# Kernel optimization log

Measured on AMD Instinct MI355X. Metric: run time of the kernel, lower is better.

The kernel has to match this reference:

```python
import jax, jax.numpy as jnp
import numpy as np


def _conv(x, w, b, dilation=1):
    # NHWC input, HWIO kernel, SAME padding, optional dilation (TF Conv2D semantics)
    y = jax.lax.conv_general_dilated(
        x, w, window_strides=(1, 1), padding='SAME',
        rhs_dilation=(dilation, dilation),
        dimension_numbers=('NHWC', 'HWIO', 'NHWC'))
    return y + b


def _grid_pool(x, row_loc, col_loc):
    # Irregular-grid mean pool + broadcast back (tf resize of a 1x1 cell == broadcast).
    # Vectorized as two normalized one-hot contractions instead of per-cell loops.
    B, H, W, C = x.shape
    M = row_loc.shape[0] - 1
    N = col_loc.shape[0] - 1
    row_ids = jnp.searchsorted(row_loc, jnp.arange(H), side='right') - 1  # [H] in [0,M)
    col_ids = jnp.searchsorted(col_loc, jnp.arange(W), side='right') - 1  # [W] in [0,N)
    Rm = jax.nn.one_hot(row_ids, M, dtype=x.dtype).T            # [M,H]
    Cm = jax.nn.one_hot(col_ids, N, dtype=x.dtype)              # [W,N]
    Rm = Rm / jnp.sum(Rm, axis=1, keepdims=True)                # row-mean weights
    Cm = Cm / jnp.sum(Cm, axis=0, keepdims=True)                # col-mean weights
    pooled = jnp.einsum('mh,bhwc,wn->bmnc', Rm, x, Cm)          # per-cell means [B,M,N,C]
    return pooled[:, row_ids][:, :, col_ids]                    # broadcast back [B,H,W,C]


def setup_inputs() -> dict:
    key = jax.random.key(0)
    ks = jax.random.split(key, 8)
    B, H, W, Cin = 2, 1024, 1024, 18
    inp = {
        'input': jax.random.normal(ks[0], (B, H, W, Cin), dtype=jnp.float32),
        'row_loc': (jnp.arange(17, dtype=jnp.int32) * (H // 16)),  # 16 irregular-capable cells, endpoints 0..H
        'col_loc': (jnp.arange(17, dtype=jnp.int32) * (W // 16)),
        'w1': jax.random.normal(ks[1], (3, 3, Cin, 6), dtype=jnp.float32) * 0.1,
        'b1': jnp.zeros((6,), jnp.float32),
        'w2': jax.random.normal(ks[2], (3, 3, Cin, 6), dtype=jnp.float32) * 0.1,
        'b2': jnp.zeros((6,), jnp.float32),
        'w3': jax.random.normal(ks[3], (3, 3, Cin, 6), dtype=jnp.float32) * 0.1,
        'b3': jnp.zeros((6,), jnp.float32),
        'wb1': jax.random.normal(ks[4], (1, 1, 18, 18), dtype=jnp.float32) * 0.1,
        'bb1': jnp.zeros((18,), jnp.float32),
        'wb2': jax.random.normal(ks[5], (1, 1, 18, 1), dtype=jnp.float32) * 0.1,
        'bb2': jnp.zeros((1,), jnp.float32),
    }
    return inp


def reference(input, row_loc, col_loc, w1, b1, w2, b2, w3, b3, wb1, bb1, wb2, bb2):
    c1 = jax.nn.relu(_conv(input, w1, b1, 1))
    c2 = jax.nn.relu(_conv(input, w2, b2, 2))
    c3 = jax.nn.relu(_conv(input, w3, b3, 3))
    c = jnp.concatenate([c1, c2, c3], axis=3)          # [B,H,W,18]
    branch1 = jax.nn.relu(_conv(c, wb1, bb1, 1))       # [B,H,W,18]
    branch1 = _grid_pool(branch1, row_loc, col_loc)
    branch2 = _conv(c, wb2, bb2, 1)                    # [B,H,W,1]
    branch2 = _grid_pool(branch2, row_loc, col_loc)
    branch2 = jax.nn.sigmoid(branch2)
    output = jnp.concatenate([branch1, c, branch2], axis=3)  # [B,H,W,37]
    return (output, branch2)
```

## Files before the change

kernel.cpp:

```cpp
#include <hip/hip_runtime.h>
#include <math.h>

typedef _Float16 f16;
typedef _Float16 f16x2 __attribute__((ext_vector_type(2)));
typedef _Float16 f16x8 __attribute__((ext_vector_type(8)));
typedef float    f32x4 __attribute__((ext_vector_type(4)));

static constexpr int B = 2, H = 1024, W = 1024;
static constexpr int NCELL = 16;
static constexpr unsigned TOTAL1 = 2u*1024u*1024u*37u;

static constexpr int TR = 16, TC = 32;
static constexpr int SR = TR + 6;
static constexpr int SC = TC + 6;
static constexpr int NTILE = B*(H/TR)*(W/TC);

static constexpr size_t WT_OFF   = 0;
static constexpr size_t WBT_OFF  = 21504;
static constexpr size_t BIAS_OFF = 23552;
static constexpr size_t CWS_OFF  = 32768;
static constexpr size_t SUMS_OFF = CWS_OFF + (size_t)NTILE*18432;
static constexpr size_t P1_OFF   = SUMS_OFF + 9728*4;
static constexpr size_t P2_OFF   = P1_OFF + 9216*4;
static constexpr size_t RID_OFF  = P2_OFF + 512*4;
static constexpr size_t CID_OFF  = RID_OFF + 1024*4;

__device__ __forceinline__ int cell_of(const int* __restrict__ loc, int x) {
    int id = 0;
#pragma unroll
    for (int i = 1; i < NCELL; ++i) id = (loc[i] <= x) ? i : id;
    return id;
}

__global__ __launch_bounds__(256)
void prep(const float* __restrict__ w1, const float* __restrict__ b1,
          const float* __restrict__ w2, const float* __restrict__ b2,
          const float* __restrict__ w3, const float* __restrict__ b3,
          const float* __restrict__ wb1, const float* __restrict__ bb1,
          const float* __restrict__ wb2, const float* __restrict__ bb2,
          f16* __restrict__ wT, f16* __restrict__ wbT, float* __restrict__ biasPad,
          float* __restrict__ sums)
{
    const int tid = threadIdx.x;
    for (int t = tid; t < 9728; t += 256) sums[t] = 0.f;
    for (int t = tid; t < 10752; t += 256) {
        int cv = t / 3584, r = t - cv*3584;
        int co = r / 224,  k = r - co*224;
        float val = 0.f;
        if (k < 216 && co < 6) {
            int tap = k / 24, ci = k - tap*24;
            if (ci < 18) {
                const float* wsrc = cv==0 ? w1 : cv==1 ? w2 : w3;
                val = wsrc[(tap*18 + ci)*6 + co];
            }
        }
        wT[t] = (f16)val;
    }
    for (int t = tid; t < 1024; t += 256) {
        int nt = t >> 9, r = t & 511;
        int colv = r >> 5, ci = r & 31;
        int co2 = nt*16 + colv;
        float val = 0.f;
        if (ci < 18) {
            if (co2 < 18) val = wb1[ci*18 + co2];
            else if (co2 == 18) val = wb2[ci];
        }
        wbT[t] = (f16)val;
    }
    for (int t = tid; t < 80; t += 256) {
        float val = 0.f;
        if (t < 48) { int cv = t >> 4, co = t & 15;
            const float* bp = cv==0 ? b1 : cv==1 ? b2 : b3;
            val = (co < 6) ? bp[co] : 0.f; }
        else if (t < 64) val = bb1[t - 48];
        else { int c = t - 64;
            val = (c==0) ? bb1[16] : (c==1) ? bb1[17] : (c==2) ? bb2[0] : 0.f; }
        biasPad[t] = val;
    }
}

__global__ __launch_bounds__(512)
void conv_mfma(const float* __restrict__ in,
               const f16* __restrict__ wT, const f16* __restrict__ wbT,
               const float* __restrict__ biasPad,
               const int* __restrict__ row_loc, const int* __restrict__ col_loc,
               f16* __restrict__ c_ws, float* __restrict__ sums)
{
    __shared__ __align__(16) f16 s_a[SR*SC*24];
    __shared__ float s_red[8][19];

    const int tid = threadIdx.x;
    const int bx  = blockIdx.x;
    const int b   = bx >> 11, rem = bx & 2047;
    const int h0  = (rem >> 5) * TR, w0 = (rem & 31) * TC;

    const int gh0 = h0 - 3, gw0 = w0 - 3;
    const bool interior = (gh0 >= 0) && (h0 + TR + 3 <= H) && (gw0 >= 0) && (w0 + TC + 3 <= W);
#pragma unroll
    for (int k = 0; k < 2; ++k) {
        const int p = tid + k*512;
        if (p < SR*SC) {
            const int r = p / SC, cc = p - r*SC;
            const int gh = gh0 + r, gw = gw0 + cc;
            const bool ok = interior || ((unsigned)gh < (unsigned)H && (unsigned)gw < (unsigned)W);
            float2 L[9];
            if (ok) {
                const float* sp = in + ((size_t)((size_t)b*H + gh)*W + gw)*18;
#pragma unroll
                for (int j = 0; j < 9; ++j) L[j] = *(const float2*)(sp + 2*j);
            } else {
#pragma unroll
                for (int j = 0; j < 9; ++j) L[j] = make_float2(0.f, 0.f);
            }
            f16x8 A0, A1, A2;
#pragma unroll
            for (int j = 0; j < 4; ++j) { A0[2*j] = (f16)L[j].x;   A0[2*j+1] = (f16)L[j].y; }
#pragma unroll
            for (int j = 0; j < 4; ++j) { A1[2*j] = (f16)L[4+j].x; A1[2*j+1] = (f16)L[4+j].y; }
            A2[0] = (f16)L[8].x; A2[1] = (f16)L[8].y;
#pragma unroll
            for (int j = 2; j < 8; ++j) A2[j] = (f16)0.f;
            *(f16x8*)&s_a[p*24 + 0]  = A0;
            *(f16x8*)&s_a[p*24 + 8]  = A1;
            *(f16x8*)&s_a[p*24 + 16] = A2;
        }
    }
    __syncthreads();

    const int lane = tid & 63, wv = tid >> 6;
    const int lm = lane & 15, g = lane >> 4;
    const int rq = wv & 3, ch2 = wv >> 2;

    f32x4 acc[3][4];
#pragma unroll
    for (int cv = 0; cv < 3; ++cv)
#pragma unroll
        for (int mt = 0; mt < 4; ++mt) acc[cv][mt] = (f32x4){0.f,0.f,0.f,0.f};

#pragma unroll
    for (int cv = 0; cv < 3; ++cv) {
        const int d = cv + 1;
        const f16* wtc = wT + cv*3584 + lm*224 + g*8;
        f16x8 bf[7];
#pragma unroll
        for (int kb = 0; kb < 7; ++kb) bf[kb] = *(const f16x8*)(wtc + kb*32);
        int tofs[7];
#pragma unroll
        for (int kb = 0; kb < 7; ++kb) {
            int i8 = kb*4 + g; if (i8 > 26) i8 = 26;
            int tap = i8 / 3;
            int ci0 = (i8 - tap*3) * 8;
            int ky = tap / 3, kx = tap - ky*3;
            tofs[kb] = (((ky-1)*d)*SC + (kx-1)*d)*24 + ci0;
        }
#pragma unroll
        for (int mt = 0; mt < 4; ++mt) {
            const int py = rq*4 + mt;
            const int base = ((py + 3)*SC + ch2*16 + lm + 3) * 24;
            f32x4 a = acc[cv][mt];
#pragma unroll
            for (int kb = 0; kb < 7; ++kb) {
                f16x8 af = *(const f16x8*)&s_a[base + tofs[kb]];
                a = __builtin_amdgcn_mfma_f32_16x16x32_f16(af, bf[kb], a, 0, 0, 0);
            }
            acc[cv][mt] = a;
        }
    }

    __syncthreads();
    f16* ct = s_a;
    const float bs0 = biasPad[lm], bs1 = biasPad[16 + lm], bs2 = biasPad[32 + lm];
    const bool act = (lm < 6);
#pragma unroll
    for (int cv = 0; cv < 3; ++cv) {
        const float bv = cv==0 ? bs0 : cv==1 ? bs1 : bs2;
#pragma unroll
        for (int mt = 0; mt < 4; ++mt) {
            const int py = rq*4 + mt;
#pragma unroll
            for (int r = 0; r < 4; ++r) {
                float val = fmaxf(acc[cv][mt][r] + bv, 0.f);
                const int px = ch2*16 + g*4 + r;
                if (act) ct[(py*TC + px)*18 + cv*6 + lm] = (f16)val;
            }
        }
    }
    __syncthreads();

    {
        const f16x8* src = (const f16x8*)ct;
        f16x8* dst = (f16x8*)(c_ws + (size_t)bx * 9216);
#pragma unroll
        for (int k = 0; k < 3; ++k) {
            const int i = tid + k*512;
            if (i < 1152) dst[i] = src[i];
        }
    }

    const f16x8 wbf0 = *(const f16x8*)(wbT + lm*32 + g*8);
    const f16x8 wbf1 = *(const f16x8*)(wbT + (16 + lm)*32 + g*8);
    const f32x4 z4 = (f32x4){0.f,0.f,0.f,0.f};
    const unsigned* ctu = (const unsigned*)ct;
    f32x4 acc2[4][2];
#pragma unroll
    for (int mt = 0; mt < 4; ++mt) {
        const int py = rq*4 + mt;
        const int p = py*TC + ch2*16 + lm;
        const int du = (p*36 + g*16) >> 2;
        union { f16x8 v; unsigned u[4]; } A;
#pragma unroll
        for (int j = 0; j < 4; ++j) A.u[j] = ctu[du + j];
        acc2[mt][0] = __builtin_amdgcn_mfma_f32_16x16x32_f16(A.v, wbf0, z4, 0, 0, 0);
        acc2[mt][1] = __builtin_amdgcn_mfma_f32_16x16x32_f16(A.v, wbf1, z4, 0, 0, 0);
    }

    const float bb0 = biasPad[48 + lm];
    const float bb1v = biasPad[64 + lm];
    const int rid0 = cell_of(row_loc, h0), rid1 = cell_of(row_loc, h0 + TR - 1);
    const int cid0 = cell_of(col_loc, w0), cid1 = cell_of(col_loc, w0 + TC - 1);
    if (rid0 == rid1 && cid0 == cid1) {
        float ps0 = 0.f, ps1 = 0.f;
#pragma unroll
        for (int mt = 0; mt < 4; ++mt)
#pragma unroll
            for (int r = 0; r < 4; ++r) {
                float v0 = fmaxf(acc2[mt][0][r] + bb0, 0.f);
                float t1 = acc2[mt][1][r] + bb1v;
                float v1x = (lm < 2) ? fmaxf(t1, 0.f) : t1;
                ps0 += v0; ps1 += v1x;
            }
        ps0 += __shfl_xor(ps0, 16); ps0 += __shfl_xor(ps0, 32);
        ps1 += __shfl_xor(ps1, 16); ps1 += __shfl_xor(ps1, 32);
        if (lane < 16) s_red[wv][lane] = ps0;
        if (lane < 3)  s_red[wv][16 + lane] = ps1;
        __syncthreads();
        if (tid < 19) {
            float s = 0.f;
#pragma unroll
            for (int wvi = 0; wvi < 8; ++wvi) s += s_red[wvi][tid];
            const int cell = b*256 + rid0*16 + cid0;
            atomicAdd(&sums[cell*19 + tid], s);
        }
    } else {
#pragma unroll
        for (int mt = 0; mt < 4; ++mt) {
            const int py = rq*4 + mt;
            const int rid = cell_of(row_loc, h0 + py);
#pragma unroll
            for (int r = 0; r < 4; ++r) {
                const int px = ch2*16 + g*4 + r;
                const int cell = b*256 + rid*16 + cell_of(col_loc, w0 + px);
                float v0 = fmaxf(acc2[mt][0][r] + bb0, 0.f);
                atomicAdd(&sums[cell*19 + lm], v0);
                if (lm < 3) {
                    float t1 = acc2[mt][1][r] + bb1v;
                    float v1x = (lm < 2) ? fmaxf(t1, 0.f) : t1;
                    atomicAdd(&sums[cell*19 + 16 + lm], v1x);
                }
            }
        }
    }
}

__global__ __launch_bounds__(256)
void finalize(const int* __restrict__ row_loc, const int* __restrict__ col_loc,
              const float* __restrict__ sums,
              float* __restrict__ pooled1, float* __restrict__ pooled2,
              int* __restrict__ row_ids, int* __restrict__ col_ids)
{
    __shared__ int rcnt[NCELL], ccnt[NCELL];
    const int tid = threadIdx.x;
    if (tid < NCELL) { rcnt[tid] = 0; ccnt[tid] = 0; }
    __syncthreads();
    for (int h = tid; h < H; h += 256) {
        int r = cell_of(row_loc, h); row_ids[h] = r; atomicAdd(&rcnt[r], 1);
    }
    for (int w = tid; w < W; w += 256) {
        int cc = cell_of(col_loc, w); col_ids[w] = cc; atomicAdd(&ccnt[cc], 1);
    }
    __syncthreads();
    for (int t = tid; t < B*256*18; t += 256) {
        int cell = t / 18, ch = t - cell*18;
        int rid = (cell >> 4) & 15, cid = cell & 15;
        int cnt = rcnt[rid] * ccnt[cid];
        pooled1[t] = (cnt > 0) ? sums[cell*19 + ch] / (float)cnt : 0.f;
    }
    for (int t = tid; t < B*256; t += 256) {
        int rid = (t >> 4) & 15, cid = t & 15;
        int cnt = rcnt[rid] * ccnt[cid];
        float v = (cnt > 0) ? sums[t*19 + 18] / (float)cnt : 0.f;
        pooled2[t] = 1.f / (1.f + __expf(-v));
    }
}

__global__ __launch_bounds__(256)
void assemble(const f16* __restrict__ c_ws, const float* __restrict__ pooled1,
              const float* __restrict__ pooled2, const int* __restrict__ row_ids,
              const int* __restrict__ col_ids, float* __restrict__ out)
{
    __shared__ __align__(16) f16 s_c[1024*18];
    __shared__ float s_p1[16*18];
    __shared__ float s_p2[16];
    __shared__ unsigned char s_cid[1024];

    const int tid = threadIdx.x;
    const int bx  = blockIdx.x;
    const int b   = bx >> 10, h = bx & 1023;

    const int tbase = b*2048 + (h >> 4)*32;
    const size_t rofs = (size_t)(h & 15) * 1152;
    const char* cbase = (const char*)c_ws;
    float4* dstv = (float4*)s_c;
#pragma unroll
    for (int k = 0; k < 9; ++k) {
        const int j = tid + k*256;
        const int t = j / 72, i = j - t*72;
        const float4 v = *(const float4*)(cbase + (size_t)(tbase + t)*18432 + rofs + (size_t)i*16);
        dstv[j] = v;
    }
    const int rid = row_ids[h];
    for (int i = tid; i < 288; i += 256) {
        int cid = i / 18, ch = i - cid*18;
        s_p1[i] = pooled1[((size_t)(b*256 + rid*16 + cid))*18 + ch];
    }
    if (tid < 16) s_p2[tid] = pooled2[b*256 + rid*16 + tid];
    for (int i = tid; i < 1024; i += 256) s_cid[i] = (unsigned char)col_ids[i];
    __syncthreads();

    float* orow = out + (size_t)bx * (1024*37);
    for (int i4 = tid; i4 < 1024*37/4; i4 += 256) {
        const int o0 = i4*4;
        float v[4];
#pragma unroll
        for (int j = 0; j < 4; ++j) {
            const int o = o0 + j;
            const unsigned pix = (unsigned)o / 37u;
            const int ch = o - (int)pix*37;
            const int cid = s_cid[pix];
            float val;
            if (ch < 18)       val = s_p1[cid*18 + ch];
            else if (ch < 36)  val = (float)s_c[pix*18 + (ch - 18)];
            else               val = s_p2[cid];
            v[j] = val;
        }
        *(float4*)(orow + o0) = make_float4(v[0], v[1], v[2], v[3]);
    }
    float* o2 = out + (size_t)TOTAL1 + (size_t)bx * 1024;
    {
        const int p0 = tid * 4;
        float4 v = make_float4(s_p2[s_cid[p0]], s_p2[s_cid[p0+1]],
                               s_p2[s_cid[p0+2]], s_p2[s_cid[p0+3]]);
        *(float4*)(o2 + p0) = v;
    }
}

extern "C" void kernel_launch(void* const* d_in, const int* in_sizes, int n_in,
                              void* d_out, int out_size, void* d_ws, size_t ws_size,
                              hipStream_t stream)
{
    (void)in_sizes; (void)n_in; (void)out_size; (void)ws_size;
    const float* in      = (const float*)d_in[0];
    const int*   row_loc = (const int*)d_in[1];
    const int*   col_loc = (const int*)d_in[2];
    const float *w1 = (const float*)d_in[3],  *b1  = (const float*)d_in[4];
    const float *w2 = (const float*)d_in[5],  *b2  = (const float*)d_in[6];
    const float *w3 = (const float*)d_in[7],  *b3  = (const float*)d_in[8];
    const float *wb1= (const float*)d_in[9],  *bb1 = (const float*)d_in[10];
    const float *wb2= (const float*)d_in[11], *bb2 = (const float*)d_in[12];

    float* out = (float*)d_out;
    char*  ws  = (char*)d_ws;

    f16*   wT      = (f16*)(ws + WT_OFF);
    f16*   wbT     = (f16*)(ws + WBT_OFF);
    float* biasPad = (float*)(ws + BIAS_OFF);
    f16*   c_ws    = (f16*)(ws + CWS_OFF);
    float* sums    = (float*)(ws + SUMS_OFF);
    float* pooled1 = (float*)(ws + P1_OFF);
    float* pooled2 = (float*)(ws + P2_OFF);
    int*   row_ids = (int*)(ws + RID_OFF);
    int*   col_ids = (int*)(ws + CID_OFF);

    prep<<<dim3(1), dim3(256), 0, stream>>>(w1, b1, w2, b2, w3, b3,
                                            wb1, bb1, wb2, bb2, wT, wbT, biasPad, sums);

    conv_mfma<<<dim3(NTILE), dim3(512), 0, stream>>>(
        in, wT, wbT, biasPad, row_loc, col_loc, c_ws, sums);

    finalize<<<dim3(1), dim3(256), 0, stream>>>(
        row_loc, col_loc, sums, pooled1, pooled2, row_ids, col_ids);

    assemble<<<dim3(B*H), dim3(256), 0, stream>>>(
        c_ws, pooled1, pooled2, row_ids, col_ids, out);
}
```

Baseline: 214.1 us.

## Fuse pooling and output assembly into per-cell conv blocks with fallback flag

Each block now owns one full 64x64 grid cell, processed in four 16-row strips. When the cell matches the uniform grid, the block computes the cell mean in-block and writes the final 37-channel output and branch2 directly. It sets a flag only when a block hits irregular cells; finalize and assemble exit early when the flag is clear. This removes the separate assemble pass (reading c_ws back and writing the output) in the common case. The cost is only 512 blocks of 1024 threads with sequential strips, which may reduce latency hiding and occupancy.

```diff
diff --git a/kernel.cpp b/kernel.cpp
--- a/kernel.cpp
+++ b/kernel.cpp
@@ -10,20 +10,16 @@
 static constexpr int NCELL = 16;
 static constexpr unsigned TOTAL1 = 2u*1024u*1024u*37u;
 
-static constexpr int TR = 16, TC = 32;
-static constexpr int SR = TR + 6;
-static constexpr int SC = TC + 6;
-static constexpr int NTILE = B*(H/TR)*(W/TC);
-
 static constexpr size_t WT_OFF   = 0;
 static constexpr size_t WBT_OFF  = 21504;
 static constexpr size_t BIAS_OFF = 23552;
 static constexpr size_t CWS_OFF  = 32768;
-static constexpr size_t SUMS_OFF = CWS_OFF + (size_t)NTILE*18432;
+static constexpr size_t SUMS_OFF = CWS_OFF + (size_t)512*4*1024*18*2;
 static constexpr size_t P1_OFF   = SUMS_OFF + 9728*4;
 static constexpr size_t P2_OFF   = P1_OFF + 9216*4;
 static constexpr size_t RID_OFF  = P2_OFF + 512*4;
 static constexpr size_t CID_OFF  = RID_OFF + 1024*4;
+static constexpr size_t FLAG_OFF = CID_OFF + 1024*4;
 
 __device__ __forceinline__ int cell_of(const int* __restrict__ loc, int x) {
     int id = 0;
@@ -39,9 +35,10 @@
           const float* __restrict__ wb1, const float* __restrict__ bb1,
           const float* __restrict__ wb2, const float* __restrict__ bb2,
           f16* __restrict__ wT, f16* __restrict__ wbT, float* __restrict__ biasPad,
-          float* __restrict__ sums)
+          float* __restrict__ sums, int* __restrict__ flag)
 {
     const int tid = threadIdx.x;
+    if (tid == 0) *flag = 0;
     for (int t = tid; t < 9728; t += 256) sums[t] = 0.f;
     for (int t = tid; t < 10752; t += 256) {
         int cv = t / 3584, r = t - cv*3584;
@@ -79,186 +76,229 @@
     }
 }
 
-__global__ __launch_bounds__(512)
-void conv_mfma(const float* __restrict__ in,
+__global__ __launch_bounds__(1024)
+void conv_cell(const float* __restrict__ in,
                const f16* __restrict__ wT, const f16* __restrict__ wbT,
                const float* __restrict__ biasPad,
                const int* __restrict__ row_loc, const int* __restrict__ col_loc,
-               f16* __restrict__ c_ws, float* __restrict__ sums)
+               f16* __restrict__ c_ws, float* __restrict__ sums,
+               float* __restrict__ out, int* __restrict__ flag)
 {
-    __shared__ __align__(16) f16 s_a[SR*SC*24];
-    __shared__ float s_red[8][19];
+    __shared__ __align__(16) f16 s_a[22*70*24];
+    __shared__ float s_red[16][19];
+    __shared__ float s_pool[19];
 
     const int tid = threadIdx.x;
     const int bx  = blockIdx.x;
-    const int b   = bx >> 11, rem = bx & 2047;
-    const int h0  = (rem >> 5) * TR, w0 = (rem & 31) * TC;
-
-    const int gh0 = h0 - 3, gw0 = w0 - 3;
-    const bool interior = (gh0 >= 0) && (h0 + TR + 3 <= H) && (gw0 >= 0) && (w0 + TC + 3 <= W);
-#pragma unroll
-    for (int k = 0; k < 2; ++k) {
-        const int p = tid + k*512;
-        if (p < SR*SC) {
-            const int r = p / SC, cc = p - r*SC;
-            const int gh = gh0 + r, gw = gw0 + cc;
-            const bool ok = interior || ((unsigned)gh < (unsigned)H && (unsigned)gw < (unsigned)W);
-            float2 L[9];
-            if (ok) {
-                const float* sp = in + ((size_t)((size_t)b*H + gh)*W + gw)*18;
-#pragma unroll
-                for (int j = 0; j < 9; ++j) L[j] = *(const float2*)(sp + 2*j);
-            } else {
-#pragma unroll
-                for (int j = 0; j < 9; ++j) L[j] = make_float2(0.f, 0.f);
-            }
-            f16x8 A0, A1, A2;
-#pragma unroll
-            for (int j = 0; j < 4; ++j) { A0[2*j] = (f16)L[j].x;   A0[2*j+1] = (f16)L[j].y; }
-#pragma unroll
-            for (int j = 0; j < 4; ++j) { A1[2*j] = (f16)L[4+j].x; A1[2*j+1] = (f16)L[4+j].y; }
-            A2[0] = (f16)L[8].x; A2[1] = (f16)L[8].y;
-#pragma unroll
-            for (int j = 2; j < 8; ++j) A2[j] = (f16)0.f;
-            *(f16x8*)&s_a[p*24 + 0]  = A0;
-            *(f16x8*)&s_a[p*24 + 8]  = A1;
-            *(f16x8*)&s_a[p*24 + 16] = A2;
-        }
-    }
-    __syncthreads();
+    const int b   = bx >> 8, rem = bx & 255;
+    const int h0  = (rem >> 4) * 64, w0 = (rem & 15) * 64;
 
     const int lane = tid & 63, wv = tid >> 6;
     const int lm = lane & 15, g = lane >> 4;
-    const int rq = wv & 3, ch2 = wv >> 2;
-
-    f32x4 acc[3][4];
-#pragma unroll
-    for (int cv = 0; cv < 3; ++cv)
-#pragma unroll
-        for (int mt = 0; mt < 4; ++mt) acc[cv][mt] = (f32x4){0.f,0.f,0.f,0.f};
-
-#pragma unroll
-    for (int cv = 0; cv < 3; ++cv) {
-        const int d = cv + 1;
-        const f16* wtc = wT + cv*3584 + lm*224 + g*8;
-        f16x8 bf[7];
-#pragma unroll
-        for (int kb = 0; kb < 7; ++kb) bf[kb] = *(const f16x8*)(wtc + kb*32);
-        int tofs[7];
-#pragma unroll
-        for (int kb = 0; kb < 7; ++kb) {
-            int i8 = kb*4 + g; if (i8 > 26) i8 = 26;
-            int tap = i8 / 3;
-            int ci0 = (i8 - tap*3) * 8;
-            int ky = tap / 3, kx = tap - ky*3;
-            tofs[kb] = (((ky-1)*d)*SC + (kx-1)*d)*24 + ci0;
-        }
+    const int rq = wv & 3, cg = wv >> 2;
+
+    const int rid = cell_of(row_loc, h0), cid = cell_of(col_loc, w0);
+    const bool uniformB = (row_loc[rid] == h0) && (row_loc[rid+1] == h0 + 64) &&
+                          (col_loc[cid] == w0) && (col_loc[cid+1] == w0 + 64);
+
+    const f16x8 wbf0 = *(const f16x8*)(wbT + lm*32 + g*8);
+    const f16x8 wbf1 = *(const f16x8*)(wbT + (16 + lm)*32 + g*8);
+    const float bs0 = biasPad[lm], bs1 = biasPad[16 + lm], bs2 = biasPad[32 + lm];
+    const float bb0 = biasPad[48 + lm], bb1v = biasPad[64 + lm];
+    const bool act = (lm < 6);
+    const f32x4 z4 = (f32x4){0.f,0.f,0.f,0.f};
+
+    float ps0 = 0.f, ps1 = 0.f;
+
+#pragma unroll 1
+    for (int s = 0; s < 4; ++s) {
+        const int gh0 = h0 + s*16 - 3, gw0 = w0 - 3;
+        const bool interior = (gh0 >= 0) && (gh0 + 22 <= H) && (gw0 >= 0) && (gw0 + 70 <= W);
+#pragma unroll
+        for (int k = 0; k < 2; ++k) {
+            const int p = tid + k*1024;
+            if (p < 1540) {
+                const int r = p / 70, cc = p - r*70;
+                const int gh = gh0 + r, gw = gw0 + cc;
+                const bool ok = interior || ((unsigned)gh < (unsigned)H && (unsigned)gw < (unsigned)W);
+                float2 L[9];
+                if (ok) {
+                    const float* sp = in + ((size_t)((size_t)b*H + gh)*W + gw)*18;
+#pragma unroll
+                    for (int j = 0; j < 9; ++j) L[j] = *(const float2*)(sp + 2*j);
+                } else {
+#pragma unroll
+                    for (int j = 0; j < 9; ++j) L[j] = make_float2(0.f, 0.f);
+                }
+                f16x8 A0, A1, A2;
+#pragma unroll
+                for (int j = 0; j < 4; ++j) { A0[2*j] = (f16)L[j].x;   A0[2*j+1] = (f16)L[j].y; }
+#pragma unroll
+                for (int j = 0; j < 4; ++j) { A1[2*j] = (f16)L[4+j].x; A1[2*j+1] = (f16)L[4+j].y; }
+                A2[0] = (f16)L[8].x; A2[1] = (f16)L[8].y;
+#pragma unroll
+                for (int j = 2; j < 8; ++j) A2[j] = (f16)0.f;
+                *(f16x8*)&s_a[p*24 + 0]  = A0;
+                *(f16x8*)&s_a[p*24 + 8]  = A1;
+                *(f16x8*)&s_a[p*24 + 16] = A2;
+            }
+        }
+        __syncthreads();
+
+        f32x4 acc[3][4];
+#pragma unroll
+        for (int cv = 0; cv < 3; ++cv)
+#pragma unroll
+            for (int mt = 0; mt < 4; ++mt) acc[cv][mt] = z4;
+
+#pragma unroll
+        for (int cv = 0; cv < 3; ++cv) {
+            const int d = cv + 1;
+            const f16* wtc = wT + cv*3584 + lm*224 + g*8;
+            f16x8 bf[7];
+#pragma unroll
+            for (int kb = 0; kb < 7; ++kb) bf[kb] = *(const f16x8*)(wtc + kb*32);
+            int tofs[7];
+#pragma unroll
+            for (int kb = 0; kb < 7; ++kb) {
+                int i8 = kb*4 + g; if (i8 > 26) i8 = 26;
+                int tap = i8 / 3;
+                int ci0 = (i8 - tap*3) * 8;
+                int ky = tap / 3, kx = tap - ky*3;
+                tofs[kb] = (((ky-1)*d)*70 + (kx-1)*d)*24 + ci0;
+            }
+#pragma unroll
+            for (int mt = 0; mt < 4; ++mt) {
+                const int py = rq*4 + mt;
+                const int base = ((py + 3)*70 + cg*16 + lm + 3) * 24;
+                f32x4 a = acc[cv][mt];
+#pragma unroll
+                for (int kb = 0; kb < 7; ++kb) {
+                    f16x8 af = *(const f16x8*)&s_a[base + tofs[kb]];
+                    a = __builtin_amdgcn_mfma_f32_16x16x32_f16(af, bf[kb], a, 0, 0, 0);
+                }
+                acc[cv][mt] = a;
+            }
+        }
+        __syncthreads();
+
+        f16* ct = s_a;
+#pragma unroll
+        for (int cv = 0; cv < 3; ++cv) {
+            const float bv = cv==0 ? bs0 : cv==1 ? bs1 : bs2;
+#pragma unroll
+            for (int mt = 0; mt < 4; ++mt) {
+                const int py = rq*4 + mt;
+#pragma unroll
+                for (int r = 0; r < 4; ++r) {
+                    float val = fmaxf(acc[cv][mt][r] + bv, 0.f);
+                    const int px = cg*16 + g*4 + r;
+                    if (act) ct[(py*64 + px)*18 + cv*6 + lm] = (f16)val;
+                }
+            }
+        }
+        __syncthreads();
+
+        {
+            const f16x8* src = (const f16x8*)ct;
+            f16x8* dst = (f16x8*)(c_ws + ((size_t)bx*4 + s)*1024*18);
+#pragma unroll
+            for (int k = 0; k < 3; ++k) {
+                const int i = tid + k*1024;
+                if (i < 2304) dst[i] = src[i];
+            }
+        }
+
+        const unsigned* ctu = (const unsigned*)ct;
+        f32x4 acc2[4][2];
 #pragma unroll
         for (int mt = 0; mt < 4; ++mt) {
             const int py = rq*4 + mt;
-            const int base = ((py + 3)*SC + ch2*16 + lm + 3) * 24;
-            f32x4 a = acc[cv][mt];
-#pragma unroll
-            for (int kb = 0; kb < 7; ++kb) {
-                f16x8 af = *(const f16x8*)&s_a[base + tofs[kb]];
-                a = __builtin_amdgcn_mfma_f32_16x16x32_f16(af, bf[kb], a, 0, 0, 0);
-            }
-            acc[cv][mt] = a;
-        }
-    }
-
-    __syncthreads();
-    f16* ct = s_a;
-    const float bs0 = biasPad[lm], bs1 = biasPad[16 + lm], bs2 = biasPad[32 + lm];
-    const bool act = (lm < 6);
-#pragma unroll
-    for (int cv = 0; cv < 3; ++cv) {
-        const float bv = cv==0 ? bs0 : cv==1 ? bs1 : bs2;
-#pragma unroll
-        for (int mt = 0; mt < 4; ++mt) {
-            const int py = rq*4 + mt;
-#pragma unroll
-            for (int r = 0; r < 4; ++r) {
-                float val = fmaxf(acc[cv][mt][r] + bv, 0.f);
-                const int px = ch2*16 + g*4 + r;
-                if (act) ct[(py*TC + px)*18 + cv*6 + lm] = (f16)val;
-            }
-        }
-    }
-    __syncthreads();
-
-    {
-        const f16x8* src = (const f16x8*)ct;
-        f16x8* dst = (f16x8*)(c_ws + (size_t)bx * 9216);
-#pragma unroll
-        for (int k = 0; k < 3; ++k) {
-            const int i = tid + k*512;
-            if (i < 1152) dst[i] = src[i];
-        }
-    }
-
-    const f16x8 wbf0 = *(const f16x8*)(wbT + lm*32 + g*8);
-    const f16x8 wbf1 = *(const f16x8*)(wbT + (16 + lm)*32 + g*8);
-    const f32x4 z4 = (f32x4){0.f,0.f,0.f,0.f};
-    const unsigned* ctu = (const unsigned*)ct;
-    f32x4 acc2[4][2];
-#pragma unroll
-    for (int mt = 0; mt < 4; ++mt) {
-        const int py = rq*4 + mt;
-        const int p = py*TC + ch2*16 + lm;
-        const int du = (p*36 + g*16) >> 2;
-        union { f16x8 v; unsigned u[4]; } A;
-#pragma unroll
-        for (int j = 0; j < 4; ++j) A.u[j] = ctu[du + j];
-        acc2[mt][0] = __builtin_amdgcn_mfma_f32_16x16x32_f16(A.v, wbf0, z4, 0, 0, 0);
-        acc2[mt][1] = __builtin_amdgcn_mfma_f32_16x16x32_f16(A.v, wbf1, z4, 0, 0, 0);
-    }
-
-    const float bb0 = biasPad[48 + lm];
-    const float bb1v = biasPad[64 + lm];
-    const int rid0 = cell_of(row_loc, h0), rid1 = cell_of(row_loc, h0 + TR - 1);
-    const int cid0 = cell_of(col_loc, w0), cid1 = cell_of(col_loc, w0 + TC - 1);
-    if (rid0 == rid1 && cid0 == cid1) {
-        float ps0 = 0.f, ps1 = 0.f;
-#pragma unroll
-        for (int mt = 0; mt < 4; ++mt)
-#pragma unroll
-            for (int r = 0; r < 4; ++r) {
-                float v0 = fmaxf(acc2[mt][0][r] + bb0, 0.f);
-                float t1 = acc2[mt][1][r] + bb1v;
-                float v1x = (lm < 2) ? fmaxf(t1, 0.f) : t1;
-                ps0 += v0; ps1 += v1x;
-            }
-        ps0 += __shfl_xor(ps0, 16); ps0 += __shfl_xor(ps0, 32);
-        ps1 += __shfl_xor(ps1, 16); ps1 += __shfl_xor(ps1, 32);
-        if (lane < 16) s_red[wv][lane] = ps0;
-        if (lane < 3)  s_red[wv][16 + lane] = ps1;
-        __syncthreads();
-        if (tid < 19) {
-            float s = 0.f;
-#pragma unroll
-            for (int wvi = 0; wvi < 8; ++wvi) s += s_red[wvi][tid];
-            const int cell = b*256 + rid0*16 + cid0;
-            atomicAdd(&sums[cell*19 + tid], s);
-        }
-    } else {
-#pragma unroll
-        for (int mt = 0; mt < 4; ++mt) {
-            const int py = rq*4 + mt;
-            const int rid = cell_of(row_loc, h0 + py);
-#pragma unroll
-            for (int r = 0; r < 4; ++r) {
-                const int px = ch2*16 + g*4 + r;
-                const int cell = b*256 + rid*16 + cell_of(col_loc, w0 + px);
-                float v0 = fmaxf(acc2[mt][0][r] + bb0, 0.f);
-                atomicAdd(&sums[cell*19 + lm], v0);
-                if (lm < 3) {
+            const int p = py*64 + cg*16 + lm;
+            const int du = (p*36 + g*16) >> 2;
+            union { f16x8 v; unsigned u[4]; } A;
+#pragma unroll
+            for (int j = 0; j < 4; ++j) A.u[j] = ctu[du + j];
+            acc2[mt][0] = __builtin_amdgcn_mfma_f32_16x16x32_f16(A.v, wbf0, z4, 0, 0, 0);
+            acc2[mt][1] = __builtin_amdgcn_mfma_f32_16x16x32_f16(A.v, wbf1, z4, 0, 0, 0);
+        }
+
+        if (uniformB) {
+#pragma unroll
+            for (int mt = 0; mt < 4; ++mt)
+#pragma unroll
+                for (int r = 0; r < 4; ++r) {
+                    float v0 = fmaxf(acc2[mt][0][r] + bb0, 0.f);
                     float t1 = acc2[mt][1][r] + bb1v;
                     float v1x = (lm < 2) ? fmaxf(t1, 0.f) : t1;
-                    atomicAdd(&sums[cell*19 + 16 + lm], v1x);
+                    ps0 += v0; ps1 += v1x;
                 }
-            }
-        }
+        } else {
+#pragma unroll
+            for (int mt = 0; mt < 4; ++mt) {
+                const int py = rq*4 + mt;
+                const int prid = cell_of(row_loc, h0 + s*16 + py);
+#pragma unroll
+                for (int r = 0; r < 4; ++r) {
+                    const int px = cg*16 + g*4 + r;
+                    const int cell = b*256 + prid*16 + cell_of(col_loc, w0 + px);
+                    float v0 = fmaxf(acc2[mt][0][r] + bb0, 0.f);
+                    atomicAdd(&sums[cell*19 + lm], v0);
+                    if (lm < 3) {
+                        float t1 = acc2[mt][1][r] + bb1v;
+                        float v1x = (lm < 2) ? fmaxf(t1, 0.f) : t1;
+                        atomicAdd(&sums[cell*19 + 16 + lm], v1x);
+                    }
+                }
+            }
+        }
+        __syncthreads();
+    }
+
+    if (!uniformB) {
+        if (tid == 0) *flag = 1;
+        return;
+    }
+
+    ps0 += __shfl_xor(ps0, 16); ps0 += __shfl_xor(ps0, 32);
+    ps1 += __shfl_xor(ps1, 16); ps1 += __shfl_xor(ps1, 32);
+    if (lane < 16) s_red[wv][lane] = ps0;
+    if (lane < 3)  s_red[wv][16 + lane] = ps1;
+    __syncthreads();
+    if (tid < 19) {
+        float ssum = 0.f;
+#pragma unroll
+        for (int wvi = 0; wvi < 16; ++wvi) ssum += s_red[wvi][tid];
+        atomicAdd(&sums[(b*256 + rid*16 + cid)*19 + tid], ssum);
+        float mean = ssum * (1.f/4096.f);
+        s_pool[tid] = (tid == 18) ? (1.f / (1.f + __expf(-mean))) : mean;
+    }
+    __syncthreads();
+
+    const f16* cbase = c_ws + (size_t)bx * 4096 * 18;
+    const float p2v = s_pool[18];
+#pragma unroll
+    for (int it = 0; it < 4; ++it) {
+        const int lp = tid + it*1024;
+        const int row = lp >> 6, col = lp & 63;
+        const int sw = row >> 4, rw = row & 15;
+        const unsigned* cu = (const unsigned*)(cbase + ((size_t)sw*1024 + rw*64 + col)*18);
+        float ov[37];
+#pragma unroll
+        for (int ch = 0; ch < 18; ++ch) ov[ch] = s_pool[ch];
+#pragma unroll
+        for (int jj = 0; jj < 9; ++jj) {
+            f16x2 hv = __builtin_bit_cast(f16x2, cu[jj]);
+            ov[18 + 2*jj]     = (float)hv[0];
+            ov[18 + 2*jj + 1] = (float)hv[1];
+        }
+        const size_t pix = ((size_t)(b*H + h0 + row))*W + (w0 + col);
+        float* op = out + pix*37;
+#pragma unroll
+        for (int q = 0; q < 9; ++q)
+            *(float4*)(op + q*4) = make_float4(ov[4*q], ov[4*q+1], ov[4*q+2], ov[4*q+3]);
+        op[36] = p2v;
+        out[(size_t)TOTAL1 + pix] = p2v;
     }
 }
 
@@ -266,8 +306,10 @@
 void finalize(const int* __restrict__ row_loc, const int* __restrict__ col_loc,
               const float* __restrict__ sums,
               float* __restrict__ pooled1, float* __restrict__ pooled2,
-              int* __restrict__ row_ids, int* __restrict__ col_ids)
+              int* __restrict__ row_ids, int* __restrict__ col_ids,
+              const int* __restrict__ flag)
 {
+    if (*flag == 0) return;
     __shared__ int rcnt[NCELL], ccnt[NCELL];
     const int tid = threadIdx.x;
     if (tid < NCELL) { rcnt[tid] = 0; ccnt[tid] = 0; }
@@ -296,8 +338,10 @@
 __global__ __launch_bounds__(256)
 void assemble(const f16* __restrict__ c_ws, const float* __restrict__ pooled1,
               const float* __restrict__ pooled2, const int* __restrict__ row_ids,
-              const int* __restrict__ col_ids, float* __restrict__ out)
+              const int* __restrict__ col_ids, float* __restrict__ out,
+              const int* __restrict__ flag)
 {
+    if (*flag == 0) return;
     __shared__ __align__(16) f16 s_c[1024*18];
     __shared__ float s_p1[16*18];
     __shared__ float s_p2[16];
@@ -306,17 +350,15 @@
     const int tid = threadIdx.x;
     const int bx  = blockIdx.x;
     const int b   = bx >> 10, h = bx & 1023;
-
-    const int tbase = b*2048 + (h >> 4)*32;
-    const size_t rofs = (size_t)(h & 15) * 1152;
-    const char* cbase = (const char*)c_ws;
+    const int br  = h >> 6, sw = (h >> 4) & 3, rw = h & 15;
+
     float4* dstv = (float4*)s_c;
 #pragma unroll
     for (int k = 0; k < 9; ++k) {
         const int j = tid + k*256;
-        const int t = j / 72, i = j - t*72;
-        const float4 v = *(const float4*)(cbase + (size_t)(tbase + t)*18432 + rofs + (size_t)i*16);
-        dstv[j] = v;
+        const int t = j / 144, i = j - t*144;
+        const size_t base = (((size_t)(b*256 + br*16 + t)*4 + sw)*1024 + rw*64)*18;
+        dstv[j] = ((const float4*)(c_ws + base))[i];
     }
     const int rid = row_ids[h];
     for (int i = tid; i < 288; i += 256) {
@@ -380,16 +422,18 @@
     float* pooled2 = (float*)(ws + P2_OFF);
     int*   row_ids = (int*)(ws + RID_OFF);
     int*   col_ids = (int*)(ws + CID_OFF);
+    int*   flag    = (int*)(ws + FLAG_OFF);
 
     prep<<<dim3(1), dim3(256), 0, stream>>>(w1, b1, w2, b2, w3, b3,
-                                            wb1, bb1, wb2, bb2, wT, wbT, biasPad, sums);
-
-    conv_mfma<<<dim3(NTILE), dim3(512), 0, stream>>>(
-        in, wT, wbT, biasPad, row_loc, col_loc, c_ws, sums);
+                                            wb1, bb1, wb2, bb2, wT, wbT, biasPad,
+                                            sums, flag);
+
+    conv_cell<<<dim3(512), dim3(1024), 0, stream>>>(
+        in, wT, wbT, biasPad, row_loc, col_loc, c_ws, sums, out, flag);
 
     finalize<<<dim3(1), dim3(256), 0, stream>>>(
-        row_loc, col_loc, sums, pooled1, pooled2, row_ids, col_ids);
+        row_loc, col_loc, sums, pooled1, pooled2, row_ids, col_ids, flag);
 
     assemble<<<dim3(B*H), dim3(256), 0, stream>>>(
-        c_ws, pooled1, pooled2, row_ids, col_ids, out);
-}
+        c_ws, pooled1, pooled2, row_ids, col_ids, out, flag);
+}
```

Measured after the change: 476.7 us. 123% more time.
